# Optimization experiments

Hardware: AMD Instinct MI355X
Metric: run time of the kernel (lower is better)

Reference implementation:

```python
import jax, jax.numpy as jnp
import numpy as np

B, N, EMB, H, C = 1, 4096, 256, 4, 64  # heads*C == 256 feeds Linear(256, EMB)
NEG_SLOPE = 0.2
LN_EPS = 1e-5


def setup_inputs() -> dict:
    key = jax.random.key(0)
    ks = jax.random.split(key, 8)
    x = jax.random.normal(ks[0], (B, N, EMB), jnp.float32)
    adj = jax.random.randint(ks[1], (B, N, N), 0, 2, jnp.int32)
    W_lin = jax.random.normal(ks[2], (EMB, H * C), jnp.float32) * (1.0 / EMB) ** 0.5
    att_src = jax.random.normal(ks[3], (H, C), jnp.float32) * 0.1
    att_dst = jax.random.normal(ks[4], (H, C), jnp.float32) * 0.1
    bias_att = jax.random.normal(ks[5], (H * C,), jnp.float32) * 0.02
    W_out = jax.random.normal(ks[6], (H * C, EMB), jnp.float32) * (1.0 / (H * C)) ** 0.5
    b_out = jax.random.normal(ks[7], (EMB,), jnp.float32) * 0.02
    gamma = jnp.ones((EMB,), jnp.float32)
    beta = jnp.zeros((EMB,), jnp.float32)
    return dict(x=x, adj=adj, W_lin=W_lin, att_src=att_src, att_dst=att_dst,
                bias_att=bias_att, W_out=W_out, b_out=b_out, gamma=gamma, beta=beta)


def reference(x, adj, W_lin, att_src, att_dst, bias_att, W_out, b_out, gamma, beta):
    # DenseGATConv (concat=True, add_loop=True, negative_slope=0.2)
    h = (x @ W_lin).reshape(B, N, H, C)                       # [B,N,H,C]
    a_src = jnp.einsum('bnhc,hc->bnh', h, att_src)            # per source node j
    a_dst = jnp.einsum('bnhc,hc->bnh', h, att_dst)            # per dest node i
    # alpha[b,i,j,h] = a_src[b,j,h] + a_dst[b,i,h]
    alpha = a_src[:, None, :, :] + a_dst[:, :, None, :]       # [B,N,N,H]
    alpha = jnp.where(alpha >= 0, alpha, NEG_SLOPE * alpha)   # leaky_relu
    # add self-loops to adjacency, then mask and softmax over source axis j
    idx = jnp.arange(N)
    adj_sl = adj.at[:, idx, idx].set(1)
    alpha = jnp.where(adj_sl[..., None] == 0, -jnp.inf, alpha)
    alpha = jax.nn.softmax(alpha, axis=2)                     # [B,N,N,H]
    out = jnp.einsum('bijh,bjhc->bihc', alpha, h)             # aggregate sources
    out = out.reshape(B, N, H * C) + bias_att                 # concat heads + GAT bias
    # trailing Linear + LayerNorm
    y = out @ W_out + b_out                                   # [B,N,EMB]
    mu = jnp.mean(y, axis=-1, keepdims=True)
    var = jnp.mean((y - mu) ** 2, axis=-1, keepdims=True)
    return (y - mu) * jax.lax.rsqrt(var + LN_EPS) * gamma + beta
```

## Files before the change

### kernel.cpp

```cpp
#include <hip/hip_runtime.h>
#include <stdint.h>

#define N    4096
#define EMB  256
#define NH   4
#define HC   64
#define PAD  40
#define LOG2E 1.4426950408889634f

typedef __attribute__((ext_vector_type(8))) short s16x8;
typedef __attribute__((ext_vector_type(4))) short s16x4;
typedef __attribute__((ext_vector_type(4))) float f32x4;
typedef __attribute__((ext_vector_type(4))) int   i32x4;
typedef unsigned short ushort_t;

__device__ __forceinline__ unsigned short f2bf(float f) {
  unsigned int u = __builtin_bit_cast(unsigned int, f);
  u += 0x7fffu + ((u >> 16) & 1u);
  return (unsigned short)(u >> 16);
}

__global__ __launch_bounds__(256)
void k_prep(const float* __restrict__ W0, ushort_t* __restrict__ WP0,
            const float* __restrict__ W1, ushort_t* __restrict__ WP1,
            const int* __restrict__ adj, unsigned int* __restrict__ abits)
{
  int b = blockIdx.x;
  if (b < 4096) {
    const int i = b;
    const int t = threadIdx.x;
    const int* src = adj + (size_t)i * N + t * 16;
    i32x4 v0 = *(const i32x4*)(src);
    i32x4 v1 = *(const i32x4*)(src + 4);
    i32x4 v2 = *(const i32x4*)(src + 8);
    i32x4 v3 = *(const i32x4*)(src + 12);
    unsigned int m = 0;
    #pragma unroll
    for (int u = 0; u < 4; ++u) {
      m |= (v0[u] != 0 ? 1u : 0u) << u;
      m |= (v1[u] != 0 ? 1u : 0u) << (4 + u);
      m |= (v2[u] != 0 ? 1u : 0u) << (8 + u);
      m |= (v3[u] != 0 ? 1u : 0u) << (12 + u);
    }
    if ((i >> 4) == t) m |= 1u << (i & 15);
    unsigned int partner = __shfl_xor(m, 1);
    if ((t & 1) == 0) {
      unsigned int word = m | (partner << 16);
      abits[(size_t)(t >> 1) * N + i] = word;
    }
  } else {
    b -= 4096;
    int k = b & 255;
    int m = threadIdx.x;
    size_t dst = ((size_t)(k >> 5) * 256 + m) * 32 + (k & 31);
    if (b < 256) WP0[dst] = f2bf(W0[k * EMB + m]);
    else         WP1[dst] = f2bf(W1[k * EMB + m]);
  }
}

__global__ __launch_bounds__(256, 4)
void k1_gemm_h(const float* __restrict__ x,
               const ushort_t* __restrict__ WlP,
               const float* __restrict__ att_src,
               const float* __restrict__ att_dst,
               ushort_t* __restrict__ hS,
               float* __restrict__ a_srcT,
               float* __restrict__ a_dstT)
{
  __shared__ ushort_t T_lds[64][20];
  __shared__ float red_lds[2][4][16];
  const int t = threadIdx.x;
  const int lane = t & 63;
  const int w = t >> 6;
  const int i0 = blockIdx.x * 16;
  const int head = blockIdx.y;
  const int c0 = head * 64;
  const int lq = lane >> 4, lm = lane & 15;

  f32x4 acc = f32x4{0.f, 0.f, 0.f, 0.f};

  const float* xrow = x + (size_t)(i0 + lm) * EMB + lq * 8;
  const ushort_t* wp = WlP + (size_t)(c0 + w * 16 + lm) * 32 + lq * 8;

  #pragma unroll 2
  for (int kp = 0; kp < 8; ++kp) {
    f32x4 v0 = *(const f32x4*)(xrow + kp * 32);
    f32x4 v1 = *(const f32x4*)(xrow + kp * 32 + 4);
    s16x8 a;
    a[0]=(short)f2bf(v0[0]); a[1]=(short)f2bf(v0[1]); a[2]=(short)f2bf(v0[2]); a[3]=(short)f2bf(v0[3]);
    a[4]=(short)f2bf(v1[0]); a[5]=(short)f2bf(v1[1]); a[6]=(short)f2bf(v1[2]); a[7]=(short)f2bf(v1[3]);
    s16x8 b = *(const s16x8*)(wp + (size_t)kp * 8192);
    acc = __builtin_amdgcn_mfma_f32_16x16x32_bf16(a, b, acc, 0, 0, 0);
  }

  float ps[4], pd[4];
  {
    int c = w * 16 + lm;
    float wsv = att_src[c0 + c];
    float wdv = att_dst[c0 + c];
    #pragma unroll
    for (int r = 0; r < 4; ++r) {
      float v = acc[r];
      T_lds[c][lq * 4 + r] = f2bf(v);
      ps[r] = v * wsv;
      pd[r] = v * wdv;
    }
  }
  #pragma unroll
  for (int r = 0; r < 4; ++r) {
    #pragma unroll
    for (int mm = 1; mm < 16; mm <<= 1) {
      ps[r] += __shfl_xor(ps[r], mm);
      pd[r] += __shfl_xor(pd[r], mm);
    }
  }
  if (lm == 0) {
    #pragma unroll
    for (int r = 0; r < 4; ++r) {
      int node = lq * 4 + r;
      red_lds[0][w][node] = ps[r];
      red_lds[1][w][node] = pd[r];
    }
  }
  __syncthreads();
  if (t < 16) {
    float s = red_lds[0][0][t] + red_lds[0][1][t] + red_lds[0][2][t] + red_lds[0][3][t];
    float d = red_lds[1][0][t] + red_lds[1][1][t] + red_lds[1][2][t] + red_lds[1][3][t];
    a_srcT[head * N + i0 + t] = s * LOG2E;
    a_dstT[head * N + i0 + t] = d * LOG2E;
  }
  {
    int c = t >> 2, seg = t & 3;
    s16x4 v = *(const s16x4*)&T_lds[c][seg * 4];
    size_t base = (((size_t)head * 128 + (i0 >> 5)) * 64 + c) * 32
                + (i0 & 16) + seg * 4;
    *(s16x4*)(hS + base) = v;
  }
}

__global__ __launch_bounds__(512, 4)
void k34_attn(const unsigned int* __restrict__ abits,
              const ushort_t* __restrict__ hS,
              const float* __restrict__ a_srcT,
              const float* __restrict__ a_dstT,
              const float* __restrict__ bias_att,
              ushort_t* __restrict__ oS)
{
  __shared__ float acc_lds[8][32][66];
  __shared__ float l_lds[8][32];

  const int t = threadIdx.x;
  const int lane = t & 63;
  const int jq = t >> 6;
  const int bid = blockIdx.x;
  const int head = (bid & 7) >> 1;
  const int i0 = (((bid >> 3) << 1) | (bid & 1)) * 32;
  const int lm = lane & 15, lq = lane >> 4;

  const float* asrc_h = a_srcT + head * N;
  const ushort_t* hS_h = hS + (size_t)head * 128 * 64 * 32;
  float ad[2];
  #pragma unroll
  for (int s = 0; s < 2; ++s) ad[s] = a_dstT[head * N + i0 + s * 16 + lm];

  s16x8 ones;
  #pragma unroll
  for (int u = 0; u < 8; ++u) ones[u] = (short)0x3f80;

  f32x4 acc[2][4];
  f32x4 accl[2];
  #pragma unroll
  for (int s = 0; s < 2; ++s) {
    accl[s] = f32x4{0.f, 0.f, 0.f, 0.f};
    #pragma unroll
    for (int nf = 0; nf < 4; ++nf) acc[s][nf] = f32x4{0.f, 0.f, 0.f, 0.f};
  }

  #pragma unroll 2
  for (int it = 0; it < 16; ++it) {
    const int jw = jq * 16 + it;
    const int jl = jw * 32 + lq * 8;

    const ushort_t* tile = hS_h + (size_t)jw * 2048;
    s16x8 b0 = *(const s16x8*)(tile + ( 0 + lm) * 32 + lq * 8);
    s16x8 b1 = *(const s16x8*)(tile + (16 + lm) * 32 + lq * 8);
    s16x8 b2 = *(const s16x8*)(tile + (32 + lm) * 32 + lq * 8);
    s16x8 b3 = *(const s16x8*)(tile + (48 + lm) * 32 + lq * 8);

    unsigned int word[2];
    #pragma unroll
    for (int s = 0; s < 2; ++s)
      word[s] = abits[(size_t)jw * N + i0 + s * 16 + lm];
    f32x4 as0 = *(const f32x4*)(asrc_h + jl);
    f32x4 as1 = *(const f32x4*)(asrc_h + jl + 4);

    #pragma unroll
    for (int s = 0; s < 2; ++s) {
      const unsigned int wsh = word[s] >> (lq * 8);
      unsigned int e[8];
      #pragma unroll
      for (int jj = 0; jj < 8; ++jj) {
        float asv = (jj < 4) ? as0[jj] : as1[jj - 4];
        float sc = asv + ad[s];
        sc = fmaxf(sc, 0.2f * sc);
        bool con = (wsh >> jj) & 1u;
        float v = con ? __builtin_amdgcn_exp2f(sc) : 0.f;
        e[jj] = __builtin_bit_cast(unsigned int, v);
      }
      i32x4 pk;
      #pragma unroll
      for (int u = 0; u < 4; ++u)
        pk[u] = (int)__builtin_amdgcn_perm(e[2 * u + 1], e[2 * u], 0x07060302u);
      s16x8 af = __builtin_bit_cast(s16x8, pk);
      __builtin_amdgcn_s_setprio(1);
      acc[s][0] = __builtin_amdgcn_mfma_f32_16x16x32_bf16(af, b0, acc[s][0], 0, 0, 0);
      acc[s][1] = __builtin_amdgcn_mfma_f32_16x16x32_bf16(af, b1, acc[s][1], 0, 0, 0);
      acc[s][2] = __builtin_amdgcn_mfma_f32_16x16x32_bf16(af, b2, acc[s][2], 0, 0, 0);
      acc[s][3] = __builtin_amdgcn_mfma_f32_16x16x32_bf16(af, b3, acc[s][3], 0, 0, 0);
      accl[s]   = __builtin_amdgcn_mfma_f32_16x16x32_bf16(af, ones, accl[s], 0, 0, 0);
      __builtin_amdgcn_s_setprio(0);
    }
  }

  #pragma unroll
  for (int s = 0; s < 2; ++s)
    #pragma unroll
    for (int nf = 0; nf < 4; ++nf)
      #pragma unroll
      for (int r = 0; r < 4; ++r)
        acc_lds[jq][s * 16 + lq * 4 + r][nf * 16 + lm] = acc[s][nf][r];
  if (lm == 0) {
    #pragma unroll
    for (int s = 0; s < 2; ++s)
      #pragma unroll
      for (int r = 0; r < 4; ++r)
        l_lds[jq][s * 16 + lq * 4 + r] = accl[s][r];
  }
  __syncthreads();

  {
    const int c = lane;
    const float bia = bias_att[head * 64 + c];
    const int nf = c >> 4;
    #pragma unroll
    for (int rr = 0; rr < 4; ++rr) {
      const int gr = jq * 4 + rr;
      float lsum = l_lds[0][gr];
      #pragma unroll
      for (int q = 1; q < 8; ++q) lsum += l_lds[q][gr];
      float v = acc_lds[0][gr][c];
      #pragma unroll
      for (int q = 1; q < 8; ++q) v += acc_lds[q][gr][c];
      const int s = gr >> 4;
      size_t idx = (((size_t)((i0 >> 4) + s) * 8) + head * 2 + (nf >> 1)) * 512
                 + (gr & 15) * 32 + (nf & 1) * 16 + (c & 15);
      oS[idx] = f2bf(v * (1.f / lsum) + bia);
    }
  }
}

__global__ __launch_bounds__(512, 2)
void k5_gemm_ln(const ushort_t* __restrict__ oS,
                const ushort_t* __restrict__ WoP,
                const float* __restrict__ b_out,
                const float* __restrict__ gamma,
                const float* __restrict__ beta,
                float* __restrict__ out)
{
  __shared__ float y_lds[16][260];
  const int t = threadIdx.x, lane = t & 63, w = t >> 6;
  const int i0 = blockIdx.x * 16;
  const int lq = lane >> 4, lm = lane & 15;

  f32x4 acc[2];
  acc[0] = f32x4{0.f, 0.f, 0.f, 0.f};
  acc[1] = f32x4{0.f, 0.f, 0.f, 0.f};

  const ushort_t* oS_b = oS + (size_t)(i0 >> 4) * 4096 + lm * 32 + lq * 8;
  const ushort_t* wp0 = WoP + (size_t)(w * 32 +  0 + lm) * 32 + lq * 8;
  const ushort_t* wp1 = WoP + (size_t)(w * 32 + 16 + lm) * 32 + lq * 8;

  #pragma unroll 2
  for (int kp = 0; kp < 8; ++kp) {
    s16x8 a  = *(const s16x8*)(oS_b + (size_t)kp * 512);
    s16x8 b0 = *(const s16x8*)(wp0 + (size_t)kp * 8192);
    s16x8 b1 = *(const s16x8*)(wp1 + (size_t)kp * 8192);
    acc[0] = __builtin_amdgcn_mfma_f32_16x16x32_bf16(a, b0, acc[0], 0, 0, 0);
    acc[1] = __builtin_amdgcn_mfma_f32_16x16x32_bf16(a, b1, acc[1], 0, 0, 0);
  }
  #pragma unroll
  for (int nf = 0; nf < 2; ++nf)
    #pragma unroll
    for (int r = 0; r < 4; ++r) {
      int row = lq * 4 + r;
      int col = w * 32 + nf * 16 + lm;
      y_lds[row][col] = acc[nf][r] + b_out[col];
    }
  __syncthreads();
  f32x4 g  = *(const f32x4*)(gamma + lane * 4);
  f32x4 be = *(const f32x4*)(beta + lane * 4);
  #pragma unroll
  for (int rr = 0; rr < 2; ++rr) {
    int r = w * 2 + rr;
    f32x4 v = *(const f32x4*)&y_lds[r][lane * 4];
    float s1 = v[0] + v[1] + v[2] + v[3];
    float s2 = v[0]*v[0] + v[1]*v[1] + v[2]*v[2] + v[3]*v[3];
    #pragma unroll
    for (int mm = 1; mm < 64; mm <<= 1) { s1 += __shfl_xor(s1, mm); s2 += __shfl_xor(s2, mm); }
    float mu = s1 * (1.f / 256.f);
    float var = s2 * (1.f / 256.f) - mu * mu;
    float rs = rsqrtf(var + 1e-5f);
    f32x4 o;
    #pragma unroll
    for (int u = 0; u < 4; ++u) o[u] = (v[u] - mu) * rs * g[u] + be[u];
    *(f32x4*)(out + (size_t)(i0 + r) * EMB + lane * 4) = o;
  }
}

extern "C" void kernel_launch(void* const* d_in, const int* in_sizes, int n_in,
                              void* d_out, int out_size, void* d_ws, size_t ws_size,
                              hipStream_t stream)
{
  (void)in_sizes; (void)n_in; (void)out_size; (void)ws_size;
  const float* x        = (const float*)d_in[0];
  const int*   adj      = (const int*)d_in[1];
  const float* W_lin    = (const float*)d_in[2];
  const float* att_src  = (const float*)d_in[3];
  const float* att_dst  = (const float*)d_in[4];
  const float* bias_att = (const float*)d_in[5];
  const float* W_out    = (const float*)d_in[6];
  const float* b_out    = (const float*)d_in[7];
  const float* gamma    = (const float*)d_in[8];
  const float* beta     = (const float*)d_in[9];
  float* out = (float*)d_out;

  uint8_t* p = (uint8_t*)d_ws;
  ushort_t* WlP = (ushort_t*)p;  p += (size_t)EMB * EMB * sizeof(ushort_t);
  ushort_t* WoP = (ushort_t*)p;  p += (size_t)EMB * EMB * sizeof(ushort_t);
  ushort_t* hS  = (ushort_t*)p;  p += (size_t)NH * HC * N * sizeof(ushort_t);
  float* a_srcb = (float*)p;     p += (size_t)NH * N * sizeof(float);
  float* a_dstb = (float*)p;     p += (size_t)NH * N * sizeof(float);
  ushort_t* oS  = (ushort_t*)p;  p += (size_t)N * EMB * sizeof(ushort_t);
  unsigned int* abits = (unsigned int*)p; p += (size_t)(N / 32) * N * sizeof(unsigned int);

  k_prep<<<4096 + 512, 256, 0, stream>>>(W_lin, WlP, W_out, WoP, adj, abits);
  k1_gemm_h<<<dim3(N / 16, NH), 256, 0, stream>>>(x, WlP, att_src, att_dst, hS, a_srcb, a_dstb);
  k34_attn<<<(N / 32) * NH, 512, 0, stream>>>(abits, hS, a_srcb, a_dstb, bias_att, oS);
  k5_gemm_ln<<<N / 16, 512, 0, stream>>>(oS, WoP, b_out, gamma, beta, out);
}
```

Before: 157.0 us.

## Co-schedule adjacency bit-packing with the h GEMM in one interleaved launch

Weight packing moves into a small separate kernel. The adjacency bit-packing blocks and the x@W_lin GEMM blocks are merged into one launch, with block indices interleaved so that every fourth block is a GEMM block. The goal is to overlap the bandwidth-bound adjacency read with the compute-bound GEMM and to remove a kernel boundary. The cost is a larger launch whose GEMM blocks may register-limit occupancy for the memory-bound blocks, and a 64KB dependency on the weight-prep kernel.

Measured after the change: 172.1 us. 1.1x slower.

```diff
diff --git a/kernel.cpp b/kernel.cpp
--- a/kernel.cpp
+++ b/kernel.cpp
@@ -5,7 +5,6 @@
 #define EMB  256
 #define NH   4
 #define HC   64
-#define PAD  40
 #define LOG2E 1.4426950408889634f
 
 typedef __attribute__((ext_vector_type(8))) short s16x8;
@@ -21,13 +20,43 @@
 }
 
 __global__ __launch_bounds__(256)
-void k_prep(const float* __restrict__ W0, ushort_t* __restrict__ WP0,
-            const float* __restrict__ W1, ushort_t* __restrict__ WP1,
-            const int* __restrict__ adj, unsigned int* __restrict__ abits)
+void k0_wprep(const float* __restrict__ W0, ushort_t* __restrict__ WP0,
+              const float* __restrict__ W1, ushort_t* __restrict__ WP1)
 {
   int b = blockIdx.x;
+  int k = b & 255;
+  int m = threadIdx.x;
+  size_t dst = ((size_t)(k >> 5) * 256 + m) * 32 + (k & 31);
+  if (b < 256) WP0[dst] = f2bf(W0[k * EMB + m]);
+  else         WP1[dst] = f2bf(W1[k * EMB + m]);
+}
+
+__global__ __launch_bounds__(256, 4)
+void kA_adj_gemm(const int* __restrict__ adj, unsigned int* __restrict__ abits,
+                 const float* __restrict__ x,
+                 const ushort_t* __restrict__ WlP,
+                 const float* __restrict__ att_src,
+                 const float* __restrict__ att_dst,
+                 ushort_t* __restrict__ hS,
+                 float* __restrict__ a_srcT,
+                 float* __restrict__ a_dstT)
+{
+  __shared__ ushort_t T_lds[64][20];
+  __shared__ float red_lds[2][4][16];
+
+  const int b = blockIdx.x;
+  bool is_k1;
+  int idx;
   if (b < 4096) {
-    const int i = b;
+    is_k1 = (b & 3) == 3;
+    idx = is_k1 ? (b >> 2) : ((b >> 2) * 3 + (b & 3));
+  } else {
+    is_k1 = false;
+    idx = 3072 + (b - 4096);
+  }
+
+  if (!is_k1) {
+    const int i = idx;
     const int t = threadIdx.x;
     const int* src = adj + (size_t)i * N + t * 16;
     i32x4 v0 = *(const i32x4*)(src);
@@ -48,32 +77,14 @@
       unsigned int word = m | (partner << 16);
       abits[(size_t)(t >> 1) * N + i] = word;
     }
-  } else {
-    b -= 4096;
-    int k = b & 255;
-    int m = threadIdx.x;
-    size_t dst = ((size_t)(k >> 5) * 256 + m) * 32 + (k & 31);
-    if (b < 256) WP0[dst] = f2bf(W0[k * EMB + m]);
-    else         WP1[dst] = f2bf(W1[k * EMB + m]);
-  }
-}
-
-__global__ __launch_bounds__(256, 4)
-void k1_gemm_h(const float* __restrict__ x,
-               const ushort_t* __restrict__ WlP,
-               const float* __restrict__ att_src,
-               const float* __restrict__ att_dst,
-               ushort_t* __restrict__ hS,
-               float* __restrict__ a_srcT,
-               float* __restrict__ a_dstT)
-{
-  __shared__ ushort_t T_lds[64][20];
-  __shared__ float red_lds[2][4][16];
+    return;
+  }
+
   const int t = threadIdx.x;
   const int lane = t & 63;
   const int w = t >> 6;
-  const int i0 = blockIdx.x * 16;
-  const int head = blockIdx.y;
+  const int i0 = (idx & 255) * 16;
+  const int head = idx >> 8;
   const int c0 = head * 64;
   const int lq = lane >> 4, lm = lane & 15;
 
@@ -89,8 +100,8 @@
     s16x8 a;
     a[0]=(short)f2bf(v0[0]); a[1]=(short)f2bf(v0[1]); a[2]=(short)f2bf(v0[2]); a[3]=(short)f2bf(v0[3]);
     a[4]=(short)f2bf(v1[0]); a[5]=(short)f2bf(v1[1]); a[6]=(short)f2bf(v1[2]); a[7]=(short)f2bf(v1[3]);
-    s16x8 b = *(const s16x8*)(wp + (size_t)kp * 8192);
-    acc = __builtin_amdgcn_mfma_f32_16x16x32_bf16(a, b, acc, 0, 0, 0);
+    s16x8 bb = *(const s16x8*)(wp + (size_t)kp * 8192);
+    acc = __builtin_amdgcn_mfma_f32_16x16x32_bf16(a, bb, acc, 0, 0, 0);
   }
 
   float ps[4], pd[4];
@@ -343,8 +354,8 @@
   ushort_t* oS  = (ushort_t*)p;  p += (size_t)N * EMB * sizeof(ushort_t);
   unsigned int* abits = (unsigned int*)p; p += (size_t)(N / 32) * N * sizeof(unsigned int);
 
-  k_prep<<<4096 + 512, 256, 0, stream>>>(W_lin, WlP, W_out, WoP, adj, abits);
-  k1_gemm_h<<<dim3(N / 16, NH), 256, 0, stream>>>(x, WlP, att_src, att_dst, hS, a_srcb, a_dstb);
+  k0_wprep<<<512, 256, 0, stream>>>(W_lin, WlP, W_out, WoP);
+  kA_adj_gemm<<<4096 + 1024, 256, 0, stream>>>(adj, abits, x, WlP, att_src, att_dst, hS, a_srcb, a_dstb);
   k34_attn<<<(N / 32) * NH, 512, 0, stream>>>(abits, hS, a_srcb, a_dstb, bias_att, oS);
   k5_gemm_ln<<<N / 16, 512, 0, stream>>>(oS, WoP, b_out, gamma, beta, out);
 }
```
